# Performance work log

Measured on AMD Instinct MI355X. Metric: run time of the kernel, lower is better.

The kernel has to match this reference:

```python
import jax, jax.numpy as jnp
import numpy as np

F, N, H = 1024, 16, 64  # features, num_heads, head_dim
B, T, S = 2, 1024, 2048  # batch, query len, memory (kv) len
M = S + 1                # relative position embeddings length


def _relative_shift(x):
    # x: [B, N, T, M] -> [B, N, T, M-1]  (Transformer-XL relative shift)
    b, h, q_len, k_len = x.shape
    x = jnp.pad(x, ((0, 0), (0, 0), (0, 0), (1, 0)))
    x = x.reshape(b, h, k_len + 1, q_len)
    x = x[:, :, 1:, :]
    x = x.reshape(b, h, q_len, k_len)
    return x[..., :-1]


def setup_inputs() -> dict:
    key = jax.random.key(0)
    ks = jax.random.split(key, 12)
    s = 1.0 / np.sqrt(F)
    return {
        'x': jax.random.normal(ks[0], (B, T, F), jnp.float32),
        'rel': jax.random.normal(ks[1], (M, F), jnp.float32),
        'memory': jax.random.normal(ks[2], (B, S, F), jnp.float32),
        'Wq': jax.random.normal(ks[3], (F, N, H), jnp.float32) * s,
        'Wk': jax.random.normal(ks[4], (F, N, H), jnp.float32) * s,
        'Wv': jax.random.normal(ks[5], (F, N, H), jnp.float32) * s,
        'Wr': jax.random.normal(ks[6], (F, N, H), jnp.float32) * s,
        'u_bias': jnp.zeros((N, H), jnp.float32),
        'v_bias': jnp.zeros((N, H), jnp.float32),
        'Wout': jax.random.normal(ks[7], (N * H, F), jnp.float32) * (1.0 / np.sqrt(N * H)),
        'b_out': jnp.zeros((F,), jnp.float32),
    }


def reference(x, rel, memory, Wq, Wk, Wv, Wr, u_bias, v_bias, Wout, b_out):
    b, t = x.shape[0], x.shape[1]
    # projections (DenseGeneral, no bias)
    q = jnp.einsum('btf,fnh->btnh', x, Wq)
    k = jnp.einsum('bsf,fnh->bsnh', memory, Wk)
    v = jnp.einsum('bsf,fnh->bsnh', memory, Wv)
    r = jnp.einsum('mf,fnh->mnh', rel, Wr)
    head_dim = q.shape[-1]
    scale = 1.0 / jnp.sqrt(jnp.asarray(head_dim, jnp.float32))
    q_u = q + u_bias[None, None]
    q_v = q + v_bias[None, None]
    # relative position bias, materialized at [B,N,T,M] then shifted
    bd = jnp.einsum('btnh,mnh->bntm', q_v, r)
    bd = _relative_shift(bd)                        # [B,N,T,S]
    bias = (bd * scale).astype(jnp.float32)
    # attention (dot_product_attention math), q/k/v in bf16 per source
    qb = q_u.astype(jnp.bfloat16)
    kb = k.astype(jnp.bfloat16)
    vb = v.astype(jnp.bfloat16)
    logits = jnp.einsum('btnh,bsnh->bnts', qb, kb).astype(jnp.float32) * scale + bias
    probs = jax.nn.softmax(logits, axis=-1)         # fp32 softmax
    out = jnp.einsum('bnts,bsnh->btnh', probs.astype(jnp.bfloat16), vb)
    out = out.astype(jnp.float32).reshape(b, t, -1)  # [B,T,N*H]
    return out @ Wout + b_out
```

## Files before the change

kernel.cpp:

```cpp
#include <hip/hip_runtime.h>
#include <cmath>

#define C_SCALE 0.18033688011112042f

typedef __attribute__((ext_vector_type(8))) short bf16x8;
typedef __attribute__((ext_vector_type(8))) _Float16 half8;
typedef __attribute__((ext_vector_type(4))) _Float16 half4;
typedef __attribute__((ext_vector_type(4))) float f32x4;
typedef __attribute__((ext_vector_type(4))) unsigned short us4;

__device__ inline unsigned short bf16_rne(float f) {
    unsigned u = __builtin_bit_cast(unsigned, f);
    u += 0x7fff + ((u >> 16) & 1);
    return (unsigned short)(u >> 16);
}

__device__ inline void lds_dma16(const _Float16* g, _Float16* l) {
    __builtin_amdgcn_global_load_lds(
        (__attribute__((address_space(1))) void*)(void*)g,
        (__attribute__((address_space(3))) void*)(void*)l, 16, 0, 0);
}

__global__ __launch_bounds__(256) void prep_kernel(
    const float* __restrict__ x, const float* __restrict__ mem,
    const float* __restrict__ rel,
    const float* __restrict__ s0, const float* __restrict__ s1,
    const float* __restrict__ s2, const float* __restrict__ s3,
    const float* __restrict__ s4,
    _Float16* __restrict__ x16, _Float16* __restrict__ mem16,
    _Float16* __restrict__ rel16,
    _Float16* __restrict__ d0, _Float16* __restrict__ d1,
    _Float16* __restrict__ d2, _Float16* __restrict__ d3,
    _Float16* __restrict__ d4)
{
    const int bx = blockIdx.x, tid = threadIdx.x;
    if (bx < 1280) {
        __shared__ _Float16 T[64][72];
        const int z = bx >> 8, rem = bx & 255;
        const float* src = z == 0 ? s0 : z == 1 ? s1 : z == 2 ? s2 : z == 3 ? s3 : s4;
        _Float16*    dst = z == 0 ? d0 : z == 1 ? d1 : z == 2 ? d2 : z == 3 ? d3 : d4;
        const int r0 = (rem & 15) * 64, c0 = (rem >> 4) * 64;
        const int r = tid >> 4, c4 = (tid & 15) * 4;
        #pragma unroll
        for (int rr = 0; rr < 64; rr += 16) {
            float4 v = *(const float4*)(src + (size_t)(r0 + r + rr) * 1024 + c0 + c4);
            T[c4 + 0][r + rr] = (_Float16)v.x;
            T[c4 + 1][r + rr] = (_Float16)v.y;
            T[c4 + 2][r + rr] = (_Float16)v.z;
            T[c4 + 3][r + rr] = (_Float16)v.w;
        }
        __syncthreads();
        const int orow = tid >> 2, seg = (tid & 3) * 16;
        half8 h0 = *(const half8*)&T[orow][seg];
        half8 h1 = *(const half8*)&T[orow][seg + 8];
        *(half8*)(dst + (size_t)(c0 + orow) * 1024 + r0 + seg)     = h0;
        *(half8*)(dst + (size_t)(c0 + orow) * 1024 + r0 + seg + 8) = h1;
    } else {
        size_t i = ((size_t)(bx - 1280) * 256 + tid) * 8;
        if (i >= 8389632ull) return;
        const float* src; _Float16* dst; size_t off;
        if (i < 2097152ull)      { src = x;   dst = x16;   off = i; }
        else if (i < 6291456ull) { src = mem; dst = mem16; off = i - 2097152ull; }
        else                     { src = rel; dst = rel16; off = i - 6291456ull; }
        float4 a = *(const float4*)(src + off);
        float4 b = *(const float4*)(src + off + 4);
        half8 h;
        h[0]=(_Float16)a.x; h[1]=(_Float16)a.y; h[2]=(_Float16)a.z; h[3]=(_Float16)a.w;
        h[4]=(_Float16)b.x; h[5]=(_Float16)b.y; h[6]=(_Float16)b.z; h[7]=(_Float16)b.w;
        *(half8*)(dst + off) = h;
    }
}

__global__ __launch_bounds__(256) void proj3_kernel(
    const _Float16* __restrict__ x16, const _Float16* __restrict__ mem16,
    const _Float16* __restrict__ rel16,
    const _Float16* __restrict__ Wqt, const _Float16* __restrict__ Wkt,
    const _Float16* __restrict__ Wvt, const _Float16* __restrict__ Wrt,
    const float* __restrict__ ub, const float* __restrict__ vb,
    unsigned short* __restrict__ qu, _Float16* __restrict__ qv,
    unsigned short* __restrict__ kb, unsigned short* __restrict__ vtb,
    _Float16* __restrict__ rb)
{
    alignas(16) __shared__ _Float16 As[128 * 64];
    alignas(16) __shared__ _Float16 Bs[128 * 64];
    const int tid = threadIdx.x;
    const int lane = tid & 63, w = tid >> 6, c = lane & 15, g = lane >> 4;
    const int bx = blockIdx.x, col0 = blockIdx.y * 128;

    int mode, row0, rowmax;
    const _Float16 *Ap, *Bp;
    if (bx < 16)      { mode = 0; row0 = bx * 128;        rowmax = 2047; Ap = x16;   Bp = Wqt; }
    else if (bx < 48) { mode = 1; row0 = (bx - 16) * 128; rowmax = 4095; Ap = mem16; Bp = Wkt; }
    else if (bx < 80) { mode = 2; row0 = (bx - 48) * 128; rowmax = 4095; Ap = mem16; Bp = Wvt; }
    else              { mode = 3; row0 = (bx - 80) * 128; rowmax = 2048; Ap = rel16; Bp = Wrt; }

    const int qr = (w & 1) * 64, qc = (w >> 1) * 64;
    const int srow = lane >> 3, phys = lane & 7;
    f32x4 acc[4][4] = {};

    for (int k0 = 0; k0 < 1024; k0 += 64) {
        #pragma unroll
        for (int q = 0; q < 4; q++) {
            int row = 32 * w + 8 * q + srow;
            int log = phys ^ (row & 7);
            int ar = row0 + row; if (ar > rowmax) ar = rowmax;
            lds_dma16(Ap + (size_t)ar * 1024 + k0 + log * 8, &As[(32 * w + 8 * q) * 64]);
            lds_dma16(Bp + (size_t)(col0 + row) * 1024 + k0 + log * 8, &Bs[(32 * w + 8 * q) * 64]);
        }
        __syncthreads();
        #pragma unroll
        for (int s = 0; s < 2; s++) {
            half8 af[4], bf[4];
            #pragma unroll
            for (int i = 0; i < 4; i++) {
                int row = qr + 16 * i + c;
                af[i] = *(const half8*)&As[row * 64 + ((4 * s + g) ^ (row & 7)) * 8];
            }
            #pragma unroll
            for (int j = 0; j < 4; j++) {
                int row = qc + 16 * j + c;
                bf[j] = *(const half8*)&Bs[row * 64 + ((4 * s + g) ^ (row & 7)) * 8];
            }
            #pragma unroll
            for (int i = 0; i < 4; i++)
                #pragma unroll
                for (int j = 0; j < 4; j++)
                    acc[i][j] = __builtin_amdgcn_mfma_f32_16x16x32_f16(af[i], bf[j], acc[i][j], 0, 0, 0);
        }
        __syncthreads();
    }

    #pragma unroll
    for (int i = 0; i < 4; i++) {
        #pragma unroll
        for (int j = 0; j < 4; j++) {
            const int cg = col0 + qc + 16 * j + c;
            const int rbase = row0 + qr + 16 * i + 4 * g;
            if (mode == 0) {
                float u = ub[cg], v = vb[cg];
                #pragma unroll
                for (int rg = 0; rg < 4; rg++) {
                    size_t o = (size_t)(rbase + rg) * 1024 + cg;
                    qu[o] = bf16_rne(acc[i][j][rg] + u);
                    qv[o] = (_Float16)((acc[i][j][rg] + v) * C_SCALE);
                }
            } else if (mode == 1) {
                #pragma unroll
                for (int rg = 0; rg < 4; rg++)
                    kb[(size_t)(rbase + rg) * 1024 + cg] = bf16_rne(acc[i][j][rg]);
            } else if (mode == 2) {
                us4 pk;
                #pragma unroll
                for (int rg = 0; rg < 4; rg++) pk[rg] = bf16_rne(acc[i][j][rg]);
                int b = rbase >> 11, s = rbase & 2047;
                *(us4*)&vtb[((size_t)(b * 16 + (cg >> 6)) * 64 + (cg & 63)) * 2048 + s] = pk;
            } else {
                #pragma unroll
                for (int rg = 0; rg < 4; rg++) {
                    int r_g = rbase + rg;
                    if (r_g < 2049)
                        rb[((size_t)(cg >> 6) * 2049 + r_g) * 64 + (cg & 63)] = (_Float16)acc[i][j][rg];
                }
            }
        }
    }
}

__global__ __launch_bounds__(256) void flash_kernel(
    const unsigned short* __restrict__ qu, const _Float16* __restrict__ qv,
    const unsigned short* __restrict__ kg, const unsigned short* __restrict__ vt,
    const _Float16* __restrict__ rb, _Float16* __restrict__ po, float* __restrict__ pl)
{
    __shared__ unsigned short Ks[64][70];
    __shared__ unsigned short Vs[64][70];
    __shared__ unsigned short Ps[64][70];
    __shared__ _Float16 BDT[128][70];
    const int tid = threadIdx.x;
    const int lane = tid & 63, w = tid >> 6, c = lane & 15, g = lane >> 4;
    const int id = blockIdx.x;
    const int p_pair = id & 127;
    const int t0 = (id >> 7) * 64;
    const int bn = p_pair >> 2, part = p_pair & 3;
    const int b = bn >> 4, n = bn & 15;
    const int s_start = part * 512;

    const unsigned short* qp = qu + (size_t)(b * 1024 + t0 + 16 * w + c) * 1024 + n * 64 + g * 8;
    bf16x8 qf0 = *(const bf16x8*)qp;
    bf16x8 qf1 = *(const bf16x8*)(qp + 32);
    const _Float16* qvp = qv + (size_t)(b * 1024 + t0 + 16 * w + c) * 1024 + n * 64 + g * 8;
    half8 av0 = *(const half8*)qvp;
    half8 av1 = *(const half8*)(qvp + 32);
    int r2 = t0 + 16 * w + c + 1; if (r2 > 1023) r2 = 1023;
    const _Float16* qvp2 = qv + (size_t)(b * 1024 + r2) * 1024 + n * 64 + g * 8;
    half8 aw0 = *(const half8*)qvp2;
    half8 aw1 = *(const half8*)(qvp2 + 32);

    const _Float16* rbase = rb + (size_t)n * 2049 * 64;

    f32x4 o[4] = {};
    float l_i[4] = {0.f, 0.f, 0.f, 0.f};

    const int sr = tid >> 2, scc = (tid & 3) * 16;
    const unsigned short* kstage = kg + (size_t)(b * 2048 + s_start + sr) * 1024 + n * 64 + scc;
    const unsigned short* vstage = vt + ((size_t)bn * 64 + sr) * 2048 + s_start + scc;

    auto r_ptr = [&](int Dl) {
        int mm = (Dl <= 1026) ? (Dl + 1023 > 2048 ? 2048 : Dl + 1023) : Dl - 1027;
        return rbase + (size_t)mm * 64 + g * 8;
    };
    auto bd_one = [&](int Dbase, int j, half8 r0, half8 r1) {
        int Dl = Dbase + 16 * j + c;
        int Dmin = Dbase + 16 * j;
        f32x4 z;
        if (Dmin + 15 <= 1026) {
            f32x4 zm = {};
            zm = __builtin_amdgcn_mfma_f32_16x16x32_f16(av0, r0, zm, 0, 0, 0);
            zm = __builtin_amdgcn_mfma_f32_16x16x32_f16(av1, r1, zm, 0, 0, 0);
            z = zm;
        } else if (Dmin >= 1027) {
            f32x4 zw = {};
            zw = __builtin_amdgcn_mfma_f32_16x16x32_f16(aw0, r0, zw, 0, 0, 0);
            zw = __builtin_amdgcn_mfma_f32_16x16x32_f16(aw1, r1, zw, 0, 0, 0);
            z = zw;
        } else {
            f32x4 zm = {}, zw = {};
            zm = __builtin_amdgcn_mfma_f32_16x16x32_f16(av0, r0, zm, 0, 0, 0);
            zm = __builtin_amdgcn_mfma_f32_16x16x32_f16(av1, r1, zm, 0, 0, 0);
            zw = __builtin_amdgcn_mfma_f32_16x16x32_f16(aw0, r0, zw, 0, 0, 0);
            zw = __builtin_amdgcn_mfma_f32_16x16x32_f16(aw1, r1, zw, 0, 0, 0);
            z = (Dl >= 1027) ? zw : zm;
        }
        if (Dl == 1026) { z[0] = 0.f; z[1] = 0.f; z[2] = 0.f; z[3] = 0.f; }
        half4 hv;
        #pragma unroll
        for (int rg = 0; rg < 4; rg++) hv[rg] = (_Float16)z[rg];
        *(half4*)&BDT[Dl & 127][16 * w + 4 * g] = hv;
    };

    const int d0 = s_start - t0;
    half8 rx[8], rr[8];
    #pragma unroll
    for (int j = 0; j < 4; j++) {
        const _Float16* rp = r_ptr(d0 - 63 + 16 * j + c);
        rx[2 * j] = *(const half8*)rp; rx[2 * j + 1] = *(const half8*)(rp + 32);
    }
    #pragma unroll
    for (int j = 0; j < 4; j++) {
        const _Float16* rp = r_ptr(d0 + 1 + 16 * j + c);
        rr[2 * j] = *(const half8*)rp; rr[2 * j + 1] = *(const half8*)(rp + 32);
    }
    uint4 k0r = *(const uint4*)(kstage);
    uint4 k1r = *(const uint4*)(kstage + 8);
    uint4 v0r = *(const uint4*)(vstage);
    uint4 v1r = *(const uint4*)(vstage + 8);

    for (int kk = 0; kk < 8; kk++) {
        const int diff0 = d0 + kk * 64;

        *(uint4*)&Ks[sr][scc]     = k0r;
        *(uint4*)&Ks[sr][scc + 8] = k1r;
        *(uint4*)&Vs[sr][scc]     = v0r;
        *(uint4*)&Vs[sr][scc + 8] = v1r;
        if (kk == 0) {
            #pragma unroll
            for (int j = 0; j < 4; j++) bd_one(d0 - 63, j, rx[2 * j], rx[2 * j + 1]);
        }
        #pragma unroll
        for (int j = 0; j < 4; j++) bd_one(diff0 + 1, j, rr[2 * j], rr[2 * j + 1]);

        __syncthreads();

        const int kn = kk < 7 ? kk + 1 : 7;
        k0r = *(const uint4*)(kstage + (size_t)(kn * 64) * 1024);
        k1r = *(const uint4*)(kstage + (size_t)(kn * 64) * 1024 + 8);
        v0r = *(const uint4*)(vstage + kn * 64);
        v1r = *(const uint4*)(vstage + kn * 64 + 8);
        const int Dn = diff0 + 65;
        #pragma unroll
        for (int j = 0; j < 4; j++) {
            const _Float16* rp = r_ptr(Dn + 16 * j + c);
            rr[2 * j] = *(const half8*)rp; rr[2 * j + 1] = *(const half8*)(rp + 32);
        }

        #pragma unroll
        for (int j = 0; j < 4; j++) {
            bf16x8 kf0 = *(const bf16x8*)&Ks[16 * j + c][g * 8];
            bf16x8 kf1 = *(const bf16x8*)&Ks[16 * j + c][32 + g * 8];
            f32x4 sa = {};
            sa = __builtin_amdgcn_mfma_f32_16x16x32_bf16(qf0, kf0, sa, 0, 0, 0);
            sa = __builtin_amdgcn_mfma_f32_16x16x32_bf16(qf1, kf1, sa, 0, 0, 0);
            #pragma unroll
            for (int rg = 0; rg < 4; rg++) {
                int tt = 16 * w + 4 * g + rg;
                int D = diff0 + 16 * j + c - tt;
                float bdt = (float)BDT[D & 127][tt];
                float p = exp2f(fmaf(sa[rg], C_SCALE, bdt));
                l_i[rg] += p;
                Ps[tt][16 * j + c] = bf16_rne(p);
            }
        }

        bf16x8 pf0 = *(const bf16x8*)&Ps[16 * w + c][g * 8];
        bf16x8 pf1 = *(const bf16x8*)&Ps[16 * w + c][32 + g * 8];
        #pragma unroll
        for (int j = 0; j < 4; j++) {
            bf16x8 vf0 = *(const bf16x8*)&Vs[16 * j + c][g * 8];
            bf16x8 vf1 = *(const bf16x8*)&Vs[16 * j + c][32 + g * 8];
            o[j] = __builtin_amdgcn_mfma_f32_16x16x32_bf16(pf0, vf0, o[j], 0, 0, 0);
            o[j] = __builtin_amdgcn_mfma_f32_16x16x32_bf16(pf1, vf1, o[j], 0, 0, 0);
        }
        __syncthreads();
    }

    #pragma unroll
    for (int rg = 0; rg < 4; rg++) {
        float s2 = l_i[rg];
        #pragma unroll
        for (int off = 1; off < 16; off <<= 1)
            s2 += __shfl_xor(s2, off, 16);
        int t = t0 + 16 * w + 4 * g + rg;
        size_t rowb = ((size_t)part * 32 + bn) * 1024 + t;
        if (c == 0) pl[rowb] = s2;
        float inv = 1.f / s2;
        #pragma unroll
        for (int j = 0; j < 4; j++)
            po[rowb * 64 + 16 * j + c] = (_Float16)(o[j][rg] * inv);
    }
}

__global__ __launch_bounds__(256) void combine_kernel(
    const _Float16* __restrict__ po, const float* __restrict__ pl,
    _Float16* __restrict__ attn)
{
    int f = blockIdx.x * 256 + threadIdx.x;
    int h = f & 63, t = (f >> 6) & 1023, bn = f >> 16;
    float os = 0.f, ls = 0.f;
    #pragma unroll
    for (int p = 0; p < 4; p++) {
        size_t rowb = ((size_t)p * 32 + bn) * 1024 + t;
        float lp = pl[rowb];
        os += lp * (float)po[rowb * 64 + h];
        ls += lp;
    }
    int b = bn >> 4, n = bn & 15;
    attn[((size_t)b * 1024 + t) * 1024 + n * 64 + h] = (_Float16)(os / ls);
}

__global__ __launch_bounds__(256) void out2_kernel(
    const _Float16* __restrict__ A, const _Float16* __restrict__ Bt,
    const float* __restrict__ bias, float* __restrict__ out)
{
    alignas(16) __shared__ _Float16 As[4096];
    alignas(16) __shared__ _Float16 Bs[4096];
    const int tid = threadIdx.x;
    const int lane = tid & 63, w = tid >> 6, c = lane & 15, g = lane >> 4;
    const int row0 = blockIdx.x * 64, col0 = blockIdx.y * 64;
    const int srow = 16 * w + (lane >> 3);
    const int phys = lane & 7;
    f32x4 acc[4] = {};

    for (int k0 = 0; k0 < 1024; k0 += 64) {
        #pragma unroll
        for (int q = 0; q < 2; q++) {
            int row = srow + 8 * q;
            int log = phys ^ (row & 7);
            lds_dma16(A  + (size_t)(row0 + row) * 1024 + k0 + log * 8, &As[(16 * w + 8 * q) * 64]);
            lds_dma16(Bt + (size_t)(col0 + row) * 1024 + k0 + log * 8, &Bs[(16 * w + 8 * q) * 64]);
        }
        __syncthreads();
        #pragma unroll
        for (int s = 0; s < 2; s++) {
            const int pc = ((4 * s + g) ^ (c & 7)) * 8;
            half8 af = *(const half8*)&As[(16 * w + c) * 64 + pc];
            #pragma unroll
            for (int j = 0; j < 4; j++) {
                half8 bf = *(const half8*)&Bs[(16 * j + c) * 64 + pc];
                acc[j] = __builtin_amdgcn_mfma_f32_16x16x32_f16(af, bf, acc[j], 0, 0, 0);
            }
        }
        __syncthreads();
    }
    #pragma unroll
    for (int j = 0; j < 4; j++)
        #pragma unroll
        for (int rg = 0; rg < 4; rg++) {
            int r_g = row0 + 16 * w + g * 4 + rg, cg = col0 + 16 * j + c;
            out[(size_t)r_g * 1024 + cg] = acc[j][rg] + bias[cg];
        }
}

extern "C" void kernel_launch(void* const* d_in, const int* in_sizes, int n_in,
                              void* d_out, int out_size, void* d_ws, size_t ws_size,
                              hipStream_t stream)
{
    const float* x    = (const float*)d_in[0];
    const float* rel  = (const float*)d_in[1];
    const float* mem  = (const float*)d_in[2];
    const float* Wq   = (const float*)d_in[3];
    const float* Wk   = (const float*)d_in[4];
    const float* Wv   = (const float*)d_in[5];
    const float* Wr   = (const float*)d_in[6];
    const float* ub   = (const float*)d_in[7];
    const float* vb   = (const float*)d_in[8];
    const float* Wout = (const float*)d_in[9];
    const float* bout = (const float*)d_in[10];
    float* out = (float*)d_out;

    char* ws = (char*)d_ws;
    unsigned short* qu    = (unsigned short*)(ws);
    _Float16*       qv    = (_Float16*)(ws + (4ull << 20));
    unsigned short* kb    = (unsigned short*)(ws + (8ull << 20));
    unsigned short* vtb   = (unsigned short*)(ws + (16ull << 20));
    _Float16*       rb    = (_Float16*)(ws + (24ull << 20));
    _Float16*       attn  = (_Float16*)(ws + (29ull << 20));
    _Float16*       po    = (_Float16*)(ws + (33ull << 20));
    float*          pl    = (float*)(ws + (50ull << 20));
    _Float16*       x16   = (_Float16*)(ws + (51ull << 20));
    _Float16*       mem16 = (_Float16*)(ws + (55ull << 20));
    _Float16*       rel16 = (_Float16*)(ws + (63ull << 20));
    _Float16*       Wqt   = (_Float16*)(ws + (68ull << 20));
    _Float16*       Wkt   = (_Float16*)(ws + (70ull << 20));
    _Float16*       Wvt   = (_Float16*)(ws + (72ull << 20));
    _Float16*       Wrt   = (_Float16*)(ws + (74ull << 20));
    _Float16*       Woutt = (_Float16*)(ws + (76ull << 20));

    prep_kernel<<<dim3(5377), 256, 0, stream>>>(
        x, mem, rel, Wq, Wk, Wv, Wr, Wout,
        x16, mem16, rel16, Wqt, Wkt, Wvt, Wrt, Woutt);
    proj3_kernel<<<dim3(97, 8), 256, 0, stream>>>(
        x16, mem16, rel16, Wqt, Wkt, Wvt, Wrt, ub, vb, qu, qv, kb, vtb, rb);
    flash_kernel<<<dim3(2048), 256, 0, stream>>>(qu, qv, kb, vtb, rb, po, pl);
    combine_kernel<<<dim3(8192), 256, 0, stream>>>(po, pl, attn);
    out2_kernel<<<dim3(32, 16), 256, 0, stream>>>(attn, Woutt, bout, out);
}
```

Before: 283.8 us.

## Load K/V fragments directly from global and drop block barriers in flash kernel

Removes the shared-memory staging of K and V tiles; each wave now loads its MFMA operand fragments straight from global memory. The QK MFMA operands are swapped so each lane holds one query row, which keeps BDT and P accesses within a single wave and lets both __syncthreads calls go. Row sums collapse to one scalar per lane and are spread with shuffles. Launch bounds now ask for 5 blocks per CU. The aim is to remove barrier stalls and raise occupancy, at the cost of four times more redundant K/V global/L2 traffic and the loss of explicit register prefetching for K, V and R.

```diff
diff --git a/kernel.cpp b/kernel.cpp
--- a/kernel.cpp
+++ b/kernel.cpp
@@ -166,13 +166,11 @@
     }
 }
 
-__global__ __launch_bounds__(256) void flash_kernel(
+__global__ __launch_bounds__(256, 5) void flash_kernel(
     const unsigned short* __restrict__ qu, const _Float16* __restrict__ qv,
     const unsigned short* __restrict__ kg, const unsigned short* __restrict__ vt,
     const _Float16* __restrict__ rb, _Float16* __restrict__ po, float* __restrict__ pl)
 {
-    __shared__ unsigned short Ks[64][70];
-    __shared__ unsigned short Vs[64][70];
     __shared__ unsigned short Ps[64][70];
     __shared__ _Float16 BDT[128][70];
     const int tid = threadIdx.x;
@@ -196,21 +194,24 @@
     half8 aw1 = *(const half8*)(qvp2 + 32);
 
     const _Float16* rbase = rb + (size_t)n * 2049 * 64;
+    const unsigned short* kbase = kg + (size_t)(b * 2048 + s_start + c) * 1024 + n * 64 + g * 8;
+    const unsigned short* vbase = vt + ((size_t)(bn * 64 + c)) * 2048 + s_start + g * 8;
 
     f32x4 o[4] = {};
-    float l_i[4] = {0.f, 0.f, 0.f, 0.f};
-
-    const int sr = tid >> 2, scc = (tid & 3) * 16;
-    const unsigned short* kstage = kg + (size_t)(b * 2048 + s_start + sr) * 1024 + n * 64 + scc;
-    const unsigned short* vstage = vt + ((size_t)bn * 64 + sr) * 2048 + s_start + scc;
+    float l_loc = 0.f;
+
+    const int d0 = s_start - t0;
 
     auto r_ptr = [&](int Dl) {
         int mm = (Dl <= 1026) ? (Dl + 1023 > 2048 ? 2048 : Dl + 1023) : Dl - 1027;
         return rbase + (size_t)mm * 64 + g * 8;
     };
-    auto bd_one = [&](int Dbase, int j, half8 r0, half8 r1) {
+    auto bd_one = [&](int Dbase, int j) {
         int Dl = Dbase + 16 * j + c;
         int Dmin = Dbase + 16 * j;
+        const _Float16* rp = r_ptr(Dl);
+        half8 r0 = *(const half8*)rp;
+        half8 r1 = *(const half8*)(rp + 32);
         f32x4 z;
         if (Dmin + 15 <= 1026) {
             f32x4 zm = {};
@@ -237,91 +238,61 @@
         *(half4*)&BDT[Dl & 127][16 * w + 4 * g] = hv;
     };
 
-    const int d0 = s_start - t0;
-    half8 rx[8], rr[8];
-    #pragma unroll
-    for (int j = 0; j < 4; j++) {
-        const _Float16* rp = r_ptr(d0 - 63 + 16 * j + c);
-        rx[2 * j] = *(const half8*)rp; rx[2 * j + 1] = *(const half8*)(rp + 32);
-    }
-    #pragma unroll
-    for (int j = 0; j < 4; j++) {
-        const _Float16* rp = r_ptr(d0 + 1 + 16 * j + c);
-        rr[2 * j] = *(const half8*)rp; rr[2 * j + 1] = *(const half8*)(rp + 32);
-    }
-    uint4 k0r = *(const uint4*)(kstage);
-    uint4 k1r = *(const uint4*)(kstage + 8);
-    uint4 v0r = *(const uint4*)(vstage);
-    uint4 v1r = *(const uint4*)(vstage + 8);
-
     for (int kk = 0; kk < 8; kk++) {
         const int diff0 = d0 + kk * 64;
 
-        *(uint4*)&Ks[sr][scc]     = k0r;
-        *(uint4*)&Ks[sr][scc + 8] = k1r;
-        *(uint4*)&Vs[sr][scc]     = v0r;
-        *(uint4*)&Vs[sr][scc + 8] = v1r;
         if (kk == 0) {
             #pragma unroll
-            for (int j = 0; j < 4; j++) bd_one(d0 - 63, j, rx[2 * j], rx[2 * j + 1]);
-        }
-        #pragma unroll
-        for (int j = 0; j < 4; j++) bd_one(diff0 + 1, j, rr[2 * j], rr[2 * j + 1]);
-
-        __syncthreads();
-
-        const int kn = kk < 7 ? kk + 1 : 7;
-        k0r = *(const uint4*)(kstage + (size_t)(kn * 64) * 1024);
-        k1r = *(const uint4*)(kstage + (size_t)(kn * 64) * 1024 + 8);
-        v0r = *(const uint4*)(vstage + kn * 64);
-        v1r = *(const uint4*)(vstage + kn * 64 + 8);
-        const int Dn = diff0 + 65;
+            for (int j = 0; j < 4; j++) bd_one(d0 - 63, j);
+        }
+        #pragma unroll
+        for (int j = 0; j < 4; j++) bd_one(diff0 + 1, j);
+
         #pragma unroll
         for (int j = 0; j < 4; j++) {
-            const _Float16* rp = r_ptr(Dn + 16 * j + c);
-            rr[2 * j] = *(const half8*)rp; rr[2 * j + 1] = *(const half8*)(rp + 32);
-        }
-
-        #pragma unroll
-        for (int j = 0; j < 4; j++) {
-            bf16x8 kf0 = *(const bf16x8*)&Ks[16 * j + c][g * 8];
-            bf16x8 kf1 = *(const bf16x8*)&Ks[16 * j + c][32 + g * 8];
+            const unsigned short* kp = kbase + (size_t)(kk * 64 + 16 * j) * 1024;
+            bf16x8 kf0 = *(const bf16x8*)kp;
+            bf16x8 kf1 = *(const bf16x8*)(kp + 32);
             f32x4 sa = {};
-            sa = __builtin_amdgcn_mfma_f32_16x16x32_bf16(qf0, kf0, sa, 0, 0, 0);
-            sa = __builtin_amdgcn_mfma_f32_16x16x32_bf16(qf1, kf1, sa, 0, 0, 0);
+            sa = __builtin_amdgcn_mfma_f32_16x16x32_bf16(kf0, qf0, sa, 0, 0, 0);
+            sa = __builtin_amdgcn_mfma_f32_16x16x32_bf16(kf1, qf1, sa, 0, 0, 0);
+            const int Dbj = diff0 + 16 * j + 4 * g - 16 * w - c;
+            us4 pk;
             #pragma unroll
             for (int rg = 0; rg < 4; rg++) {
-                int tt = 16 * w + 4 * g + rg;
-                int D = diff0 + 16 * j + c - tt;
-                float bdt = (float)BDT[D & 127][tt];
+                float bdt = (float)BDT[(Dbj + rg) & 127][16 * w + c];
                 float p = exp2f(fmaf(sa[rg], C_SCALE, bdt));
-                l_i[rg] += p;
-                Ps[tt][16 * j + c] = bf16_rne(p);
+                l_loc += p;
+                pk[rg] = bf16_rne(p);
             }
+            *(us4*)&Ps[16 * w + c][16 * j + 4 * g] = pk;
         }
 
         bf16x8 pf0 = *(const bf16x8*)&Ps[16 * w + c][g * 8];
         bf16x8 pf1 = *(const bf16x8*)&Ps[16 * w + c][32 + g * 8];
         #pragma unroll
         for (int j = 0; j < 4; j++) {
-            bf16x8 vf0 = *(const bf16x8*)&Vs[16 * j + c][g * 8];
-            bf16x8 vf1 = *(const bf16x8*)&Vs[16 * j + c][32 + g * 8];
+            const unsigned short* vp = vbase + (size_t)(16 * j) * 2048 + kk * 64;
+            bf16x8 vf0 = *(const bf16x8*)vp;
+            bf16x8 vf1 = *(const bf16x8*)(vp + 32);
             o[j] = __builtin_amdgcn_mfma_f32_16x16x32_bf16(pf0, vf0, o[j], 0, 0, 0);
             o[j] = __builtin_amdgcn_mfma_f32_16x16x32_bf16(pf1, vf1, o[j], 0, 0, 0);
         }
-        __syncthreads();
-    }
-
+    }
+
+    float s2 = l_loc;
+    s2 += __shfl_xor(s2, 16);
+    s2 += __shfl_xor(s2, 32);
+    if (g == 0) {
+        size_t rowb = ((size_t)part * 32 + bn) * 1024 + (t0 + 16 * w + c);
+        pl[rowb] = s2;
+    }
     #pragma unroll
     for (int rg = 0; rg < 4; rg++) {
-        float s2 = l_i[rg];
-        #pragma unroll
-        for (int off = 1; off < 16; off <<= 1)
-            s2 += __shfl_xor(s2, off, 16);
+        float s2r = __shfl(s2, 4 * g + rg);
+        float inv = 1.f / s2r;
         int t = t0 + 16 * w + 4 * g + rg;
         size_t rowb = ((size_t)part * 32 + bn) * 1024 + t;
-        if (c == 0) pl[rowb] = s2;
-        float inv = 1.f / s2;
         #pragma unroll
         for (int j = 0; j < 4; j++)
             po[rowb * 64 + 16 * j + c] = (_Float16)(o[j][rg] * inv);
```

New measurement: 378.0 us. +33.2%, slower.
